# Optimization experiments

Hardware: AMD Instinct MI355X
Metric: run time of the kernel (lower is better)

The kernel has to match this reference:

```python
import jax, jax.numpy as jnp
import numpy as np

B, L, D, H = 2, 128, 256, 256
BASE_LR = 0.01
LR_SHIFT = float(np.log(np.expm1(BASE_LR)))  # log(expm1(base_lr))


def silu_backward(x):
    s = jax.nn.silu(x)
    return s + jax.nn.sigmoid(x) * (1.0 - s)


def decay_matrix(log_g):
    # log_g: [B,L] -> M[b,l,m] = exp(sum_{i=m+1..l} log_g[b,i]) for m<=l, else 0
    n = log_g.shape[1]
    strict = jnp.tril(jnp.ones((n, n), log_g.dtype), -1)
    cum = jnp.cumsum(log_g[:, :, None] * strict, axis=1)
    return jnp.exp(cum) * jnp.tril(jnp.ones((n, n), log_g.dtype))


def setup_inputs():
    key = jax.random.key(0)
    ks = jax.random.split(key, 22)
    p = lambda k, shape: jax.random.normal(k, shape, jnp.float32) * 0.02
    inp = {
        'x': jax.random.normal(ks[0], (B, L, D), jnp.float32),
        'Wq': p(ks[1], (D, D)), 'bq': p(ks[2], (D,)),
        'Wk': p(ks[3], (D, D)), 'bk': p(ks[4], (D,)),
        'Wv': p(ks[5], (D, D)), 'bv': p(ks[6], (D,)),
        'Wlr': p(ks[7], (D, 1)), 'blr': p(ks[8], (1,)),
        'Wm': p(ks[9], (D, 1)), 'bm': p(ks[10], (1,)),
        'Wd': p(ks[11], (D, 1)), 'bd': p(ks[12], (1,)),
        'W1': p(ks[13], (B, H, D)), 'b1': p(ks[14], (B, H)),
        'W2': p(ks[15], (B, D, H)), 'b2': p(ks[16], (B, D)),
        'mW1': p(ks[17], (B, H, D)), 'mb1': p(ks[18], (B, H)),
        'mW2': p(ks[19], (B, D, H)), 'mb2': p(ks[20], (B, D)),
    }
    return inp


def reference(x, Wq, bq, Wk, bk, Wv, bv, Wlr, blr, Wm, bm, Wd, bd,
              W1, b1, W2, b2, mW1, mb1, mW2, mb2):
    query = x @ Wq + bq
    key_ = x @ Wk + bk
    value = x @ Wv + bv

    # forward through fast-weight MLP at current (chunk-start) weights
    Z1 = jnp.einsum('bhd,bld->blh', W1, key_) + b1[:, None, :]
    X2 = jax.nn.silu(Z1)
    Z2 = jnp.einsum('bdh,blh->bld', W2, X2) + b2[:, None, :]

    # per-token gradients of 0.5*||Z2 - value||^2
    grad_Z2 = Z2 - value
    grad_b2 = grad_Z2
    grad_W2 = jnp.einsum('bld,blh->bldh', grad_Z2, X2)
    grad_X2 = jnp.einsum('bld,bdh->blh', grad_Z2, W2)
    grad_Z1 = grad_X2 * silu_backward(Z1)
    grad_b1 = grad_Z1
    grad_W1 = jnp.einsum('blh,bld->blhd', grad_Z1, key_)

    lr = jax.nn.softplus((x @ Wlr).squeeze(-1) + blr + LR_SHIFT)  # [B,L]
    gW1 = grad_W1 * lr[:, :, None, None]
    gb1 = grad_b1 * lr[:, :, None]
    gW2 = grad_W2 * lr[:, :, None, None]
    gb2 = grad_b2 * lr[:, :, None]

    # momentum recurrence (decay-gated linear scan, materialized as LxL matrix)
    fc_mom = (x @ Wm).squeeze(-1) + bm  # [B,L]
    log_mom = -jax.nn.softplus(-fc_mom)
    M = decay_matrix(log_mom)  # [B,L,L]
    mom_cum = jnp.exp(jnp.cumsum(log_mom, axis=1))  # [B,L]

    mgW1 = jnp.einsum('blm,bmhd->blhd', M, gW1) - jnp.einsum('bl,bhd->blhd', mom_cum, mW1)
    mgb1 = jnp.einsum('blm,bmh->blh', M, gb1) - jnp.einsum('bl,bh->blh', mom_cum, mb1)
    mgW2 = jnp.einsum('blm,bmdh->bldh', M, gW2) - jnp.einsum('bl,bdh->bldh', mom_cum, mW2)
    mgb2 = jnp.einsum('blm,bmd->bld', M, gb2) - jnp.einsum('bl,bd->bld', mom_cum, mb2)

    # weight-decay recurrence
    log_wd = -jax.nn.softplus((x @ Wd).squeeze(-1) + bd)  # [B,L]
    Dm = decay_matrix(log_wd)
    wd_cum = jnp.exp(jnp.cumsum(log_wd, axis=1))

    W1p = jnp.einsum('blm,bmhd->blhd', Dm, mgW1) + jnp.einsum('bl,bhd->blhd', wd_cum, W1)
    b1p = jnp.einsum('blm,bmh->blh', Dm, mgb1) + jnp.einsum('bl,bh->blh', wd_cum, b1)
    W2p = jnp.einsum('blm,bmdh->bldh', Dm, mgW2) + jnp.einsum('bl,bdh->bldh', wd_cum, W2)
    b2p = jnp.einsum('blm,bmd->bld', Dm, mgb2) + jnp.einsum('bl,bd->bld', wd_cum, b2)

    # query pass through per-token updated weights
    Zq1 = jnp.einsum('blhd,bld->blh', W1p, query) + b1p
    Zq2 = jnp.einsum('bldh,blh->bld', W2p, jax.nn.silu(Zq1)) + b2p

    return (Zq2,
            W1p[:, -1], b1p[:, -1], W2p[:, -1], b2p[:, -1],
            mgW1[:, -1], mgb1[:, -1], mgW2[:, -1], mgb2[:, -1])
```

## Files before the change

### kernel.cpp

```cpp
#include <hip/hip_runtime.h>
#include <math.h>

constexpr int Bn = 2, Ln = 128, Dn = 256, Hn = 256;

#define LR_SHIFT (-4.6001660040607144f)

constexpr int OFF_Q      = 0;
constexpr int OFF_K      = 65536;
constexpr int OFF_V      = 131072;
constexpr int OFF_X2     = 196608;
constexpr int OFF_GZ1    = 262144;
constexpr int OFF_GZ2    = 327680;
constexpr int OFF_XQ     = 393216;
constexpr int OFF_KT     = 458752;
constexpr int OFF_A      = 524288;
constexpr int OFF_W1T    = 557056;
constexpr int OFF_W2T    = 688128;
constexpr int OFF_MW1T   = 819200;
constexpr int OFF_MW2T   = 950272;
constexpr int OFF_LR     = 1081344;
constexpr int OFF_PM     = 1081600;
constexpr int OFF_PD     = 1081856;
constexpr int OFF_MOMCUM = 1082112;
constexpr int OFF_WDCUM  = 1082368;
constexpr int OFF_C      = 1082624;
constexpr int OFF_LOGM   = 1082880;
constexpr int OFF_LOGWD  = 1083136;
constexpr int OFF_X2T    = 1083392;
constexpr int OFF_U1     = 1148928;
constexpr int OFF_V1     = 1214464;
constexpr int OFF_P1     = 1411072;

constexpr int OUT_ZQ2  = 0;
constexpr int OUT_W1P  = 65536;
constexpr int OUT_B1P  = 196608;
constexpr int OUT_W2P  = 197120;
constexpr int OUT_B2P  = 328192;
constexpr int OUT_MGW1 = 328704;
constexpr int OUT_MGB1 = 459776;
constexpr int OUT_MGW2 = 460288;
constexpr int OUT_MGB2 = 591360;

struct KParams {
    const float *x;
    const float *Wq, *bq, *Wk, *bk, *Wv, *bv;
    const float *Wlr, *blr, *Wm, *bm, *Wd, *bd;
    const float *W1, *b1, *W2, *b2, *mW1, *mb1, *mW2, *mb2;
    float *out, *ws;
};

__device__ __forceinline__ float softplus_f(float z) {
    return fmaxf(z, 0.0f) + log1pf(expf(-fabsf(z)));
}
__device__ __forceinline__ float4 fma4(float s, const float4 w, float4 a) {
    a.x += s * w.x; a.y += s * w.y; a.z += s * w.z; a.w += s * w.w; return a;
}
__device__ __forceinline__ float silu_f(float z) {
    return z / (1.0f + expf(-z));
}
__device__ __forceinline__ float dsilu_mul(float a, float z) {
    float sg = 1.0f / (1.0f + expf(-z));
    return a * (sg * (1.0f + z * (1.0f - sg)));
}

__device__ __forceinline__ void stage8(const float* __restrict__ src,
                                       float (*xs)[260], int t) {
#pragma unroll
    for (int i = 0; i < 2; ++i) {
        int e = t + i * 256; int tok = e >> 6, kq = e & 63;
        *(float4*)&xs[tok][kq * 4] = *(const float4*)(src + tok * 256 + kq * 4);
    }
}

__device__ __forceinline__ float4 dot256(const float (*xs)[260], int tok,
                                         const float* __restrict__ Wc, int ldw) {
    float4 a = {0, 0, 0, 0};
    for (int k0 = 0; k0 < 256; k0 += 16) {
        float4 wb[16];
#pragma unroll
        for (int kk = 0; kk < 16; ++kk)
            wb[kk] = *(const float4*)(Wc + (k0 + kk) * ldw);
#pragma unroll
        for (int kk = 0; kk < 16; ++kk)
            a = fma4(xs[tok][k0 + kk], wb[kk], a);
    }
    return a;
}

__device__ __forceinline__ void lastw_unit(const KParams& p, float* smem, int t,
                                           int b, int fam, int i0, int j0) {
    const float* ws = p.ws;
    float* wa = smem;
    float* wm = smem + 128;
    float (*LA)[16] = (float (*)[16])(smem + 256);
    float (*LM)[16] = (float (*)[16])(smem + 256 + 2048);
    float (*R)[16]  = (float (*)[16])(smem + 256 + 4096);
    const float* lr = ws + OFF_LR + b * Ln;
    const float* Pm = ws + OFF_PM + b * Ln;
    const float* Arow = ws + OFF_A + (b * Ln + Ln - 1) * Ln;
    if (t < 128) {
        wa[t] = Arow[t] * lr[t];
        wm[t] = expf(Pm[Ln - 1] - Pm[t]) * lr[t];
    }
    const float* left  = ws + (fam == 0 ? OFF_GZ1 : OFF_GZ2) + b * Ln * 256;
    const float* right = ws + (fam == 0 ? OFF_K   : OFF_X2 ) + b * Ln * 256;
    __syncthreads();
#pragma unroll
    for (int i = 0; i < 2; ++i) {
        int e = t + i * 256;
        int m = e >> 2, iq = (e & 3) * 4;
        float4 lv = *(const float4*)(left + m * 256 + i0 + iq);
        float4 rv = *(const float4*)(right + m * 256 + j0 + iq);
        float wam = wa[m], wmm = wm[m];
        LA[m][iq + 0] = wam * lv.x; LA[m][iq + 1] = wam * lv.y;
        LA[m][iq + 2] = wam * lv.z; LA[m][iq + 3] = wam * lv.w;
        LM[m][iq + 0] = wmm * lv.x; LM[m][iq + 1] = wmm * lv.y;
        LM[m][iq + 2] = wmm * lv.z; LM[m][iq + 3] = wmm * lv.w;
        R[m][iq + 0] = rv.x; R[m][iq + 1] = rv.y;
        R[m][iq + 2] = rv.z; R[m][iq + 3] = rv.w;
    }
    __syncthreads();
    int tx = t & 15, ty = t >> 4;
    float accA = 0.0f, accM = 0.0f;
#pragma unroll 4
    for (int m = 0; m < 128; ++m) {
        accA += LA[m][ty] * R[m][tx];
        accM += LM[m][ty] * R[m][tx];
    }
    float c_last  = ws[OFF_C + b * Ln + Ln - 1];
    float wd_last = ws[OFF_WDCUM + b * Ln + Ln - 1];
    float mc_last = ws[OFF_MOMCUM + b * Ln + Ln - 1];
    int i = i0 + ty, j = j0 + tx;
    const float* base1 = (fam == 0 ? p.W1 : p.W2) + b * 65536;
    const float* basem = (fam == 0 ? p.mW1 : p.mW2) + b * 65536;
    float b1v = base1[i * 256 + j], bmv = basem[i * 256 + j];
    int op = (fam == 0 ? OUT_W1P : OUT_W2P) + (b * 256 + i) * 256 + j;
    int om = (fam == 0 ? OUT_MGW1 : OUT_MGW2) + (b * 256 + i) * 256 + j;
    p.out[op] = accA - c_last * bmv + wd_last * b1v;
    p.out[om] = accM - mc_last * bmv;
}

__device__ __forceinline__ void score_unit(const KParams& p, float* smem, int t,
                                           int b, int l0, int srcoff, int btoff,
                                           int poff) {
    const float* ws = p.ws;
    float (*qs)[260] = (float (*)[260])smem;
    stage8(ws + srcoff + (b * 128 + l0) * 256, qs, t);
    __syncthreads();
    int tok = t >> 5, mq = t & 31, m0 = 4 * mq;
    int l = l0 + tok;
    float4 s = dot256(qs, tok, ws + btoff + b * 32768 + m0, 128);
    float4 A4 = *(const float4*)(ws + OFF_A + (b * 128 + l) * 128 + m0);
    float4 L4 = *(const float4*)(ws + OFF_LR + b * 128 + m0);
    float4 pv;
    pv.x = (m0 + 0 <= l) ? A4.x * L4.x * (1.0f + s.x) : 0.0f;
    pv.y = (m0 + 1 <= l) ? A4.y * L4.y * (1.0f + s.y) : 0.0f;
    pv.z = (m0 + 2 <= l) ? A4.z * L4.z * (1.0f + s.z) : 0.0f;
    pv.w = (m0 + 3 <= l) ? A4.w * L4.w * (1.0f + s.w) : 0.0f;
    *(float4*)(p.ws + poff + b * 16384 + l * 128 + m0) = pv;
}

__device__ __forceinline__ float4 pg_dot(const float* __restrict__ G,
                                         const float* __restrict__ prow,
                                         int mmax) {
    float4 acc = {0, 0, 0, 0};
    int m0 = 0;
    for (; m0 + 16 <= mmax; m0 += 16) {
        float4 gb[16];
#pragma unroll
        for (int kk = 0; kk < 16; ++kk)
            gb[kk] = *(const float4*)(G + (m0 + kk) * 256);
#pragma unroll
        for (int kk = 0; kk < 16; ++kk)
            acc = fma4(prow[m0 + kk], gb[kk], acc);
    }
    for (; m0 < mmax; m0 += 8) {
        float4 gb[8];
#pragma unroll
        for (int kk = 0; kk < 8; ++kk)
            gb[kk] = *(const float4*)(G + (m0 + kk) * 256);
#pragma unroll
        for (int kk = 0; kk < 8; ++kk)
            acc = fma4(prow[m0 + kk], gb[kk], acc);
    }
    return acc;
}

__global__ __launch_bounds__(256) void phase0_kernel(KParams p) {
    __shared__ float smem[4160];
    int u = blockIdx.x, t = threadIdx.x;
    float* ws = p.ws;
    if (u < 512) {
        int z = u >> 6; int mat = z >> 1; int b = z & 1;
        const float* src; float* dst;
        if (mat == 0)      { src = p.W1  + b * 65536; dst = ws + OFF_W1T  + b * 65536; }
        else if (mat == 1) { src = p.W2  + b * 65536; dst = ws + OFF_W2T  + b * 65536; }
        else if (mat == 2) { src = p.mW1 + b * 65536; dst = ws + OFF_MW1T + b * 65536; }
        else               { src = p.mW2 + b * 65536; dst = ws + OFF_MW2T + b * 65536; }
        float (*tile)[33] = (float (*)[33])smem;
        int tx = t & 31, ty = t >> 5;
        int tid = u & 63;
        int r0 = (tid >> 3) * 32, c0 = (tid & 7) * 32;
        for (int i = 0; i < 32; i += 8)
            tile[ty + i][tx] = src[(r0 + ty + i) * 256 + (c0 + tx)];
        __syncthreads();
        for (int i = 0; i < 32; i += 8)
            dst[(c0 + ty + i) * 256 + (r0 + tx)] = tile[tx][ty + i];
    } else if (u < 704) {
        int v = u - 512; int mat = v >> 6; int r = v & 63;
        int ct = r >> 5, tt = r & 31;
        int bl0 = tt * 8, c0 = ct * 128;
        const float* W    = (mat == 0) ? p.Wq : (mat == 1) ? p.Wk : p.Wv;
        const float* bias = (mat == 0) ? p.bq : (mat == 1) ? p.bk : p.bv;
        int outoff = (mat == 0) ? OFF_Q : (mat == 1) ? OFF_K : OFF_V;
        float (*xs)[260] = (float (*)[260])smem;
        stage8(p.x + bl0 * 256, xs, t);
        __syncthreads();
        int tok = t >> 5, q = t & 31;
        int c = c0 + 4 * q;
        float4 a = dot256(xs, tok, W + c, 256);
        float4 bb = *(const float4*)(bias + c);
        a.x += bb.x; a.y += bb.y; a.z += bb.z; a.w += bb.w;
        *(float4*)(ws + outoff + (bl0 + tok) * 256 + c) = a;
        if (mat == 1) {
            int b = bl0 >> 7, l = (bl0 & 127) + tok;
            float* KT = ws + OFF_KT + b * 32768 + l;
            KT[(c + 0) * 128] = a.x; KT[(c + 1) * 128] = a.y;
            KT[(c + 2) * 128] = a.z; KT[(c + 3) * 128] = a.w;
        }
    } else {
        int blk = u - 704;
        int ln = t & 63, wv = t >> 6;
        int bl = blk * 4 + wv;
        float4 xv = *(const float4*)(p.x + bl * 256 + ln * 4);
        float4 wl = *(const float4*)(p.Wlr + ln * 4);
        float4 wm = *(const float4*)(p.Wm + ln * 4);
        float4 wd = *(const float4*)(p.Wd + ln * 4);
        float s1 = xv.x * wl.x + xv.y * wl.y + xv.z * wl.z + xv.w * wl.w;
        float s2 = xv.x * wm.x + xv.y * wm.y + xv.z * wm.z + xv.w * wm.w;
        float s3 = xv.x * wd.x + xv.y * wd.y + xv.z * wd.z + xv.w * wd.w;
#pragma unroll
        for (int off = 32; off > 0; off >>= 1) {
            s1 += __shfl_xor(s1, off);
            s2 += __shfl_xor(s2, off);
            s3 += __shfl_xor(s3, off);
        }
        if (ln == 0) {
            ws[OFF_LR + bl]    = softplus_f(s1 + p.blr[0] + LR_SHIFT);
            ws[OFF_LOGM + bl]  = -softplus_f(-(s2 + p.bm[0]));
            ws[OFF_LOGWD + bl] = -softplus_f(s3 + p.bd[0]);
        }
    }
}

__global__ __launch_bounds__(256) void phase1_kernel(KParams p) {
    __shared__ float smem[4160];
    int u = blockIdx.x, t = threadIdx.x;
    float* ws = p.ws;
    if (u < 64) {
        int tt = u >> 1, ct = u & 1;
        int bl0 = tt * 8, c0 = ct * 128, b = bl0 >> 7;
        float (*xs)[260] = (float (*)[260])smem;
        stage8(ws + OFF_K + bl0 * 256, xs, t);
        __syncthreads();
        int tok = t >> 5, q = t & 31;
        int c = c0 + 4 * q;
        float4 a = dot256(xs, tok, ws + OFF_W1T + b * 65536 + c, 256);
        float4 bb = *(const float4*)(p.b1 + b * 256 + c);
        float4 z = {a.x + bb.x, a.y + bb.y, a.z + bb.z, a.w + bb.w};
        *(float4*)(ws + OFF_GZ1 + (bl0 + tok) * 256 + c) = z;
        float4 s = {silu_f(z.x), silu_f(z.y), silu_f(z.z), silu_f(z.w)};
        *(float4*)(ws + OFF_X2 + (bl0 + tok) * 256 + c) = s;
        int l = (bl0 & 127) + tok;
        float* X2T = ws + OFF_X2T + b * 32768 + l;
        X2T[(c + 0) * 128] = s.x; X2T[(c + 1) * 128] = s.y;
        X2T[(c + 2) * 128] = s.z; X2T[(c + 3) * 128] = s.w;
    } else if (u < 320) {
        int w = u - 64; int b = w >> 7; int l = w & 127;
        float* sm = smem;
        float* sd = smem + 128;
        float* se = smem + 256;
        if (t < 128) {
            sm[t] = ws[OFF_LOGM + b * Ln + t];
            sd[t] = ws[OFF_LOGWD + b * Ln + t];
        }
        __syncthreads();
        for (int off = 1; off < 128; off <<= 1) {
            float am = 0.0f, ad = 0.0f;
            if (t < 128 && t >= off) { am = sm[t - off]; ad = sd[t - off]; }
            __syncthreads();
            if (t < 128) { sm[t] += am; sd[t] += ad; }
            __syncthreads();
        }
        if (l == 0) {
            if (t < 128) {
                float pm = sm[t], pd = sd[t];
                ws[OFF_PM + b * Ln + t] = pm;
                ws[OFF_PD + b * Ln + t] = pd;
                ws[OFF_MOMCUM + b * Ln + t] = expf(pm);
                ws[OFF_WDCUM + b * Ln + t]  = expf(pd);
                se[t] = expf(pm - pd);
            }
            __syncthreads();
            for (int off = 1; off < 128; off <<= 1) {
                float a = 0.0f;
                if (t < 128 && t >= off) a = se[t - off];
                __syncthreads();
                if (t < 128) se[t] += a;
                __syncthreads();
            }
            if (t < 128) ws[OFF_C + b * Ln + t] = expf(sd[t]) * se[t];
        }
        if (t < 128) {
            int m1 = t;
            float a = 0.0f;
            if (m1 <= l) {
                float pdl = sd[l], pmm1 = sm[m1];
                float s = 0.0f;
                for (int m = m1; m <= l; ++m)
                    s += expf((pdl - sd[m]) + (sm[m] - pmm1));
                a = s;
            }
            ws[OFF_A + (b * Ln + l) * Ln + m1] = a;
        }
    } else {
        int w = u - 320; int mat = w >> 6; int r = w & 63;
        int tt = r >> 1, ct = r & 1;
        int bl0 = tt * 8, c0 = ct * 128, b = bl0 >> 7;
        float (*xs)[260] = (float (*)[260])smem;
        stage8(ws + OFF_Q + bl0 * 256, xs, t);
        __syncthreads();
        int tok = t >> 5, q = t & 31;
        int c = c0 + 4 * q;
        const float* W = ws + (mat ? OFF_MW1T : OFF_W1T) + b * 65536 + c;
        const float* bias = (mat ? p.mb1 : p.b1) + b * 256 + c;
        float4 a = dot256(xs, tok, W, 256);
        float4 bb = *(const float4*)bias;
        a.x += bb.x; a.y += bb.y; a.z += bb.z; a.w += bb.w;
        *(float4*)(ws + (mat ? OFF_V1 : OFF_U1) + (bl0 + tok) * 256 + c) = a;
    }
}

__global__ __launch_bounds__(256) void phase2_kernel(KParams p) {
    __shared__ float smem[4160];
    int u = blockIdx.x, t = threadIdx.x;
    float* ws = p.ws;
    if (u < 32) {
        int bl0 = u * 8, b = bl0 >> 7;
        float (*xs)[260] = (float (*)[260])smem;
        float (*gs)[260] = (float (*)[260])(smem + 2080);
        stage8(ws + OFF_X2 + bl0 * 256, xs, t);
        __syncthreads();
        int tok = t >> 5, q = t & 31;
        int c = 4 * q, c2 = c + 128;
        {
            const float* W2t = ws + OFF_W2T + b * 65536;
            float4 a0 = dot256(xs, tok, W2t + c, 256);
            float4 a1 = dot256(xs, tok, W2t + c2, 256);
            float4 bb0 = *(const float4*)(p.b2 + b * 256 + c);
            float4 bb1 = *(const float4*)(p.b2 + b * 256 + c2);
            float4 v0 = *(const float4*)(ws + OFF_V + (bl0 + tok) * 256 + c);
            float4 v1 = *(const float4*)(ws + OFF_V + (bl0 + tok) * 256 + c2);
            float4 g0 = {a0.x + bb0.x - v0.x, a0.y + bb0.y - v0.y,
                         a0.z + bb0.z - v0.z, a0.w + bb0.w - v0.w};
            float4 g1 = {a1.x + bb1.x - v1.x, a1.y + bb1.y - v1.y,
                         a1.z + bb1.z - v1.z, a1.w + bb1.w - v1.w};
            *(float4*)&gs[tok][c]  = g0;
            *(float4*)&gs[tok][c2] = g1;
            *(float4*)(ws + OFF_GZ2 + (bl0 + tok) * 256 + c)  = g0;
            *(float4*)(ws + OFF_GZ2 + (bl0 + tok) * 256 + c2) = g1;
        }
        __syncthreads();
        {
            const float* W2n = p.W2 + b * 65536;
            float4 a0 = dot256(gs, tok, W2n + c, 256);
            float4 a1 = dot256(gs, tok, W2n + c2, 256);
            float4 z0 = *(const float4*)(ws + OFF_GZ1 + (bl0 + tok) * 256 + c);
            float4 z1 = *(const float4*)(ws + OFF_GZ1 + (bl0 + tok) * 256 + c2);
            float4 g0 = {dsilu_mul(a0.x, z0.x), dsilu_mul(a0.y, z0.y),
                         dsilu_mul(a0.z, z0.z), dsilu_mul(a0.w, z0.w)};
            float4 g1 = {dsilu_mul(a1.x, z1.x), dsilu_mul(a1.y, z1.y),
                         dsilu_mul(a1.z, z1.z), dsilu_mul(a1.w, z1.w)};
            *(float4*)(ws + OFF_GZ1 + (bl0 + tok) * 256 + c)  = g0;
            *(float4*)(ws + OFF_GZ1 + (bl0 + tok) * 256 + c2) = g1;
        }
    } else {
        int w = u - 32; int b = w >> 4; int l0 = (w & 15) * 8;
        score_unit(p, smem, t, b, l0, OFF_Q, OFF_KT, OFF_P1);
    }
}

__global__ __launch_bounds__(256) void phase3_kernel(KParams p) {
    __shared__ float smem[6400];
    int u = blockIdx.x, t = threadIdx.x;
    float* ws = p.ws;
    if (u < 32) {
        int b = u >> 4; int l0 = (u & 15) * 8; int bl0 = b * 128 + l0;
        float (*xqs)[260] = (float (*)[260])smem;
        float (*ps)[132]  = (float (*)[132])(smem + 2080);
        {
            int tok = t >> 5, mq = t & 31;
            *(float4*)&ps[tok][mq * 4] =
                *(const float4*)(ws + OFF_P1 + b * 16384 + (l0 + tok) * 128 + mq * 4);
        }
        __syncthreads();
        int tok = t >> 5, q = t & 31;
        int l = l0 + tok;
        float cl  = ws[OFF_C + b * 128 + l];
        float wdc = ws[OFF_WDCUM + b * 128 + l];
        int mmax = l0 + 8;
#pragma unroll
        for (int half = 0; half < 2; ++half) {
            int c = half * 128 + 4 * q;
            float4 acc = pg_dot(ws + OFF_GZ1 + b * 32768 + c, ps[tok], mmax);
            float4 u4 = *(const float4*)(ws + OFF_U1 + (bl0 + tok) * 256 + c);
            float4 v4 = *(const float4*)(ws + OFF_V1 + (bl0 + tok) * 256 + c);
            float4 o;
            o.x = silu_f(acc.x - cl * v4.x + wdc * u4.x);
            o.y = silu_f(acc.y - cl * v4.y + wdc * u4.y);
            o.z = silu_f(acc.z - cl * v4.z + wdc * u4.z);
            o.w = silu_f(acc.w - cl * v4.w + wdc * u4.w);
            *(float4*)&xqs[tok][c] = o;
        }
        __syncthreads();
        {
            int mq = t & 31, m0 = 4 * mq;
            float4 s = dot256(xqs, tok, ws + OFF_X2T + b * 32768 + m0, 128);
            float4 A4 = *(const float4*)(ws + OFF_A + (b * 128 + l) * 128 + m0);
            float4 L4 = *(const float4*)(ws + OFF_LR + b * 128 + m0);
            float4 pv;
            pv.x = (m0 + 0 <= l) ? A4.x * L4.x * (1.0f + s.x) : 0.0f;
            pv.y = (m0 + 1 <= l) ? A4.y * L4.y * (1.0f + s.y) : 0.0f;
            pv.z = (m0 + 2 <= l) ? A4.z * L4.z * (1.0f + s.z) : 0.0f;
            pv.w = (m0 + 3 <= l) ? A4.w * L4.w * (1.0f + s.w) : 0.0f;
            *(float4*)&ps[tok][m0] = pv;
        }
        __syncthreads();
#pragma unroll
        for (int half = 0; half < 2; ++half) {
            int c = half * 128 + 4 * q;
            float4 uacc = dot256(xqs, tok, ws + OFF_W2T + b * 65536 + c, 256);
            float4 bb = *(const float4*)(p.b2 + b * 256 + c);
            uacc.x += bb.x; uacc.y += bb.y; uacc.z += bb.z; uacc.w += bb.w;
            float4 vacc = dot256(xqs, tok, ws + OFF_MW2T + b * 65536 + c, 256);
            float4 mb = *(const float4*)(p.mb2 + b * 256 + c);
            vacc.x += mb.x; vacc.y += mb.y; vacc.z += mb.z; vacc.w += mb.w;
            float4 acc = pg_dot(ws + OFF_GZ2 + b * 32768 + c, ps[tok], mmax);
            float4 o;
            o.x = acc.x - cl * vacc.x + wdc * uacc.x;
            o.y = acc.y - cl * vacc.y + wdc * uacc.y;
            o.z = acc.z - cl * vacc.z + wdc * uacc.z;
            o.w = acc.w - cl * vacc.w + wdc * uacc.w;
            *(float4*)(p.out + OUT_ZQ2 + (bl0 + tok) * 256 + c) = o;
        }
    } else if (u < 1056) {
        int w = u - 32; int z = w >> 8; int rem = w & 255;
        int b = z >> 1; int fam = z & 1;
        lastw_unit(p, smem, t, b, fam, (rem >> 4) * 16, (rem & 15) * 16);
    } else {
        int b = u - 1056;
        float* wa = smem;
        float* wm = smem + 128;
        if (t < 128) {
            wa[t] = ws[OFF_A + (b * Ln + Ln - 1) * Ln + t] * ws[OFF_LR + b * Ln + t];
            wm[t] = expf(ws[OFF_PM + b * Ln + Ln - 1] - ws[OFF_PM + b * Ln + t]) *
                    ws[OFF_LR + b * Ln + t];
        }
        __syncthreads();
        const float* gz1 = ws + OFF_GZ1 + b * Ln * 256;
        const float* gz2 = ws + OFF_GZ2 + b * Ln * 256;
        float sA1 = 0, sM1 = 0, sA2 = 0, sM2 = 0;
        for (int m0 = 0; m0 < 128; m0 += 16) {
            float g1b[16], g2b[16];
#pragma unroll
            for (int kk = 0; kk < 16; ++kk) {
                g1b[kk] = gz1[(m0 + kk) * 256 + t];
                g2b[kk] = gz2[(m0 + kk) * 256 + t];
            }
#pragma unroll
            for (int kk = 0; kk < 16; ++kk) {
                float wam = wa[m0 + kk], wmm = wm[m0 + kk];
                sA1 += wam * g1b[kk]; sM1 += wmm * g1b[kk];
                sA2 += wam * g2b[kk]; sM2 += wmm * g2b[kk];
            }
        }
        float c_last  = ws[OFF_C + b * Ln + Ln - 1];
        float wd_last = ws[OFF_WDCUM + b * Ln + Ln - 1];
        float mc_last = ws[OFF_MOMCUM + b * Ln + Ln - 1];
        p.out[OUT_B1P + b * 256 + t]  = sA1 - c_last * p.mb1[b * 256 + t] + wd_last * p.b1[b * 256 + t];
        p.out[OUT_MGB1 + b * 256 + t] = sM1 - mc_last * p.mb1[b * 256 + t];
        p.out[OUT_B2P + b * 256 + t]  = sA2 - c_last * p.mb2[b * 256 + t] + wd_last * p.b2[b * 256 + t];
        p.out[OUT_MGB2 + b * 256 + t] = sM2 - mc_last * p.mb2[b * 256 + t];
    }
}

extern "C" void kernel_launch(void* const* d_in, const int* in_sizes, int n_in,
                              void* d_out, int out_size, void* d_ws, size_t ws_size,
                              hipStream_t stream) {
    KParams p;
    p.x   = (const float*)d_in[0];
    p.Wq  = (const float*)d_in[1];  p.bq  = (const float*)d_in[2];
    p.Wk  = (const float*)d_in[3];  p.bk  = (const float*)d_in[4];
    p.Wv  = (const float*)d_in[5];  p.bv  = (const float*)d_in[6];
    p.Wlr = (const float*)d_in[7];  p.blr = (const float*)d_in[8];
    p.Wm  = (const float*)d_in[9];  p.bm  = (const float*)d_in[10];
    p.Wd  = (const float*)d_in[11]; p.bd  = (const float*)d_in[12];
    p.W1  = (const float*)d_in[13]; p.b1  = (const float*)d_in[14];
    p.W2  = (const float*)d_in[15]; p.b2  = (const float*)d_in[16];
    p.mW1 = (const float*)d_in[17]; p.mb1 = (const float*)d_in[18];
    p.mW2 = (const float*)d_in[19]; p.mb2 = (const float*)d_in[20];
    p.out = (float*)d_out;
    p.ws  = (float*)d_ws;

    phase0_kernel<<<768, 256, 0, stream>>>(p);
    phase1_kernel<<<448, 256, 0, stream>>>(p);
    phase2_kernel<<<64, 256, 0, stream>>>(p);
    phase3_kernel<<<1058, 256, 0, stream>>>(p);
}
```

Measured before the change: 222.4 us.

## Restructure phases: fold scans into phase0, fuse K-projection into MLP, split query pass

```diff
diff --git a/kernel.cpp b/kernel.cpp
--- a/kernel.cpp
+++ b/kernel.cpp
@@ -24,11 +24,11 @@
 constexpr int OFF_MOMCUM = 1082112;
 constexpr int OFF_WDCUM  = 1082368;
 constexpr int OFF_C      = 1082624;
-constexpr int OFF_LOGM   = 1082880;
-constexpr int OFF_LOGWD  = 1083136;
 constexpr int OFF_X2T    = 1083392;
 constexpr int OFF_U1     = 1148928;
 constexpr int OFF_V1     = 1214464;
+constexpr int OFF_U2     = 1280000;
+constexpr int OFF_V2     = 1345536;
 constexpr int OFF_P1     = 1411072;
 
 constexpr int OUT_ZQ2  = 0;
@@ -186,12 +186,118 @@
     return acc;
 }
 
+__device__ __forceinline__ void combine_unit(const KParams& p, float* smem, int t,
+                                             int b, int l0, int c0, int poff,
+                                             int goff, int uoff, int voff,
+                                             int dooutsilu, float* dst) {
+    const float* ws = p.ws;
+    int bl0 = b * 128 + l0;
+    float (*ps)[132] = (float (*)[132])smem;
+    {
+        int tok = t >> 5, mq = t & 31;
+        *(float4*)&ps[tok][mq * 4] =
+            *(const float4*)(ws + poff + b * 16384 + (l0 + tok) * 128 + mq * 4);
+    }
+    __syncthreads();
+    int tok = t >> 5, q = t & 31;
+    int l = l0 + tok;
+    int c = c0 + 4 * q;
+    float cl  = ws[OFF_C + b * 128 + l];
+    float wdc = ws[OFF_WDCUM + b * 128 + l];
+    float4 acc = pg_dot(ws + goff + b * 32768 + c, ps[tok], l0 + 8);
+    float4 u4 = *(const float4*)(ws + uoff + (bl0 + tok) * 256 + c);
+    float4 v4 = *(const float4*)(ws + voff + (bl0 + tok) * 256 + c);
+    float4 o;
+    o.x = acc.x - cl * v4.x + wdc * u4.x;
+    o.y = acc.y - cl * v4.y + wdc * u4.y;
+    o.z = acc.z - cl * v4.z + wdc * u4.z;
+    o.w = acc.w - cl * v4.w + wdc * u4.w;
+    if (dooutsilu) {
+        o.x = silu_f(o.x); o.y = silu_f(o.y); o.z = silu_f(o.z); o.w = silu_f(o.w);
+    }
+    *(float4*)(dst + (bl0 + tok) * 256 + c) = o;
+}
+
 __global__ __launch_bounds__(256) void phase0_kernel(KParams p) {
     __shared__ float smem[4160];
     int u = blockIdx.x, t = threadIdx.x;
     float* ws = p.ws;
-    if (u < 512) {
-        int z = u >> 6; int mat = z >> 1; int b = z & 1;
+    if (u < 2) {
+        int b = u;
+        float* sm = smem;
+        float* sd = smem + 128;
+        float* se = smem + 256;
+        int wv = t >> 6, ln = t & 63;
+        float4 wl = *(const float4*)(p.Wlr + ln * 4);
+        float4 wm = *(const float4*)(p.Wm + ln * 4);
+        float4 wd = *(const float4*)(p.Wd + ln * 4);
+        for (int r = 0; r < 4; ++r) {
+            float4 xr[8];
+#pragma unroll
+            for (int j = 0; j < 8; ++j) {
+                int tok = wv * 32 + r * 8 + j;
+                xr[j] = *(const float4*)(p.x + (b * 128 + tok) * 256 + ln * 4);
+            }
+#pragma unroll
+            for (int j = 0; j < 8; ++j) {
+                int tok = wv * 32 + r * 8 + j;
+                float s1 = xr[j].x * wl.x + xr[j].y * wl.y + xr[j].z * wl.z + xr[j].w * wl.w;
+                float s2 = xr[j].x * wm.x + xr[j].y * wm.y + xr[j].z * wm.z + xr[j].w * wm.w;
+                float s3 = xr[j].x * wd.x + xr[j].y * wd.y + xr[j].z * wd.z + xr[j].w * wd.w;
+#pragma unroll
+                for (int off = 32; off > 0; off >>= 1) {
+                    s1 += __shfl_xor(s1, off);
+                    s2 += __shfl_xor(s2, off);
+                    s3 += __shfl_xor(s3, off);
+                }
+                if (ln == 0) {
+                    ws[OFF_LR + b * 128 + tok] = softplus_f(s1 + p.blr[0] + LR_SHIFT);
+                    sm[tok] = -softplus_f(-(s2 + p.bm[0]));
+                    sd[tok] = -softplus_f(s3 + p.bd[0]);
+                }
+            }
+        }
+        __syncthreads();
+        for (int off = 1; off < 128; off <<= 1) {
+            float am = 0.0f, ad = 0.0f;
+            if (t < 128 && t >= off) { am = sm[t - off]; ad = sd[t - off]; }
+            __syncthreads();
+            if (t < 128) { sm[t] += am; sd[t] += ad; }
+            __syncthreads();
+        }
+        if (t < 128) {
+            float pm = sm[t], pd = sd[t];
+            ws[OFF_PM + b * Ln + t] = pm;
+            ws[OFF_PD + b * Ln + t] = pd;
+            ws[OFF_MOMCUM + b * Ln + t] = expf(pm);
+            ws[OFF_WDCUM + b * Ln + t]  = expf(pd);
+            se[t] = expf(pm - pd);
+        }
+        __syncthreads();
+        for (int off = 1; off < 128; off <<= 1) {
+            float a = 0.0f;
+            if (t < 128 && t >= off) a = se[t - off];
+            __syncthreads();
+            if (t < 128) se[t] += a;
+            __syncthreads();
+        }
+        if (t < 128) ws[OFF_C + b * Ln + t] = expf(sd[t]) * se[t];
+        __syncthreads();
+        for (int e = t; e < 16384; e += 256) {
+            int l = e >> 7, m1 = e & 127;
+            float a = 0.0f;
+            if (m1 <= l) {
+                float pdl = sd[l], pmm1 = sm[m1];
+                float s = 0.0f;
+                for (int m = m1; m <= l; ++m)
+                    s += expf((pdl - sd[m]) + (sm[m] - pmm1));
+                a = s;
+            }
+            ws[OFF_A + (b * Ln + l) * Ln + m1] = a;
+        }
+    } else if (u < 514) {
+        int w = u - 2;
+        int z = w >> 6; int mat = z >> 1; int b = z & 1;
         const float* src; float* dst;
         if (mat == 0)      { src = p.W1  + b * 65536; dst = ws + OFF_W1T  + b * 65536; }
         else if (mat == 1) { src = p.W2  + b * 65536; dst = ws + OFF_W2T  + b * 65536; }
@@ -199,15 +305,15 @@
         else               { src = p.mW2 + b * 65536; dst = ws + OFF_MW2T + b * 65536; }
         float (*tile)[33] = (float (*)[33])smem;
         int tx = t & 31, ty = t >> 5;
-        int tid = u & 63;
+        int tid = w & 63;
         int r0 = (tid >> 3) * 32, c0 = (tid & 7) * 32;
         for (int i = 0; i < 32; i += 8)
             tile[ty + i][tx] = src[(r0 + ty + i) * 256 + (c0 + tx)];
         __syncthreads();
         for (int i = 0; i < 32; i += 8)
             dst[(c0 + ty + i) * 256 + (r0 + tx)] = tile[tx][ty + i];
-    } else if (u < 704) {
-        int v = u - 512; int mat = v >> 6; int r = v & 63;
+    } else {
+        int v = u - 514; int mat = v >> 6; int r = v & 63;
         int ct = r >> 5, tt = r & 31;
         int bl0 = tt * 8, c0 = ct * 128;
         const float* W    = (mat == 0) ? p.Wq : (mat == 1) ? p.Wk : p.Wv;
@@ -228,135 +334,55 @@
             KT[(c + 0) * 128] = a.x; KT[(c + 1) * 128] = a.y;
             KT[(c + 2) * 128] = a.z; KT[(c + 3) * 128] = a.w;
         }
-    } else {
-        int blk = u - 704;
-        int ln = t & 63, wv = t >> 6;
-        int bl = blk * 4 + wv;
-        float4 xv = *(const float4*)(p.x + bl * 256 + ln * 4);
-        float4 wl = *(const float4*)(p.Wlr + ln * 4);
-        float4 wm = *(const float4*)(p.Wm + ln * 4);
-        float4 wd = *(const float4*)(p.Wd + ln * 4);
-        float s1 = xv.x * wl.x + xv.y * wl.y + xv.z * wl.z + xv.w * wl.w;
-        float s2 = xv.x * wm.x + xv.y * wm.y + xv.z * wm.z + xv.w * wm.w;
-        float s3 = xv.x * wd.x + xv.y * wd.y + xv.z * wd.z + xv.w * wd.w;
-#pragma unroll
-        for (int off = 32; off > 0; off >>= 1) {
-            s1 += __shfl_xor(s1, off);
-            s2 += __shfl_xor(s2, off);
-            s3 += __shfl_xor(s3, off);
-        }
-        if (ln == 0) {
-            ws[OFF_LR + bl]    = softplus_f(s1 + p.blr[0] + LR_SHIFT);
-            ws[OFF_LOGM + bl]  = -softplus_f(-(s2 + p.bm[0]));
-            ws[OFF_LOGWD + bl] = -softplus_f(s3 + p.bd[0]);
-        }
     }
 }
 
 __global__ __launch_bounds__(256) void phase1_kernel(KParams p) {
-    __shared__ float smem[4160];
-    int u = blockIdx.x, t = threadIdx.x;
-    float* ws = p.ws;
-    if (u < 64) {
-        int tt = u >> 1, ct = u & 1;
-        int bl0 = tt * 8, c0 = ct * 128, b = bl0 >> 7;
-        float (*xs)[260] = (float (*)[260])smem;
-        stage8(ws + OFF_K + bl0 * 256, xs, t);
-        __syncthreads();
-        int tok = t >> 5, q = t & 31;
-        int c = c0 + 4 * q;
-        float4 a = dot256(xs, tok, ws + OFF_W1T + b * 65536 + c, 256);
-        float4 bb = *(const float4*)(p.b1 + b * 256 + c);
-        float4 z = {a.x + bb.x, a.y + bb.y, a.z + bb.z, a.w + bb.w};
-        *(float4*)(ws + OFF_GZ1 + (bl0 + tok) * 256 + c) = z;
-        float4 s = {silu_f(z.x), silu_f(z.y), silu_f(z.z), silu_f(z.w)};
-        *(float4*)(ws + OFF_X2 + (bl0 + tok) * 256 + c) = s;
-        int l = (bl0 & 127) + tok;
-        float* X2T = ws + OFF_X2T + b * 32768 + l;
-        X2T[(c + 0) * 128] = s.x; X2T[(c + 1) * 128] = s.y;
-        X2T[(c + 2) * 128] = s.z; X2T[(c + 3) * 128] = s.w;
-    } else if (u < 320) {
-        int w = u - 64; int b = w >> 7; int l = w & 127;
-        float* sm = smem;
-        float* sd = smem + 128;
-        float* se = smem + 256;
-        if (t < 128) {
-            sm[t] = ws[OFF_LOGM + b * Ln + t];
-            sd[t] = ws[OFF_LOGWD + b * Ln + t];
-        }
-        __syncthreads();
-        for (int off = 1; off < 128; off <<= 1) {
-            float am = 0.0f, ad = 0.0f;
-            if (t < 128 && t >= off) { am = sm[t - off]; ad = sd[t - off]; }
-            __syncthreads();
-            if (t < 128) { sm[t] += am; sd[t] += ad; }
-            __syncthreads();
-        }
-        if (l == 0) {
-            if (t < 128) {
-                float pm = sm[t], pd = sd[t];
-                ws[OFF_PM + b * Ln + t] = pm;
-                ws[OFF_PD + b * Ln + t] = pd;
-                ws[OFF_MOMCUM + b * Ln + t] = expf(pm);
-                ws[OFF_WDCUM + b * Ln + t]  = expf(pd);
-                se[t] = expf(pm - pd);
-            }
-            __syncthreads();
-            for (int off = 1; off < 128; off <<= 1) {
-                float a = 0.0f;
-                if (t < 128 && t >= off) a = se[t - off];
-                __syncthreads();
-                if (t < 128) se[t] += a;
-                __syncthreads();
-            }
-            if (t < 128) ws[OFF_C + b * Ln + t] = expf(sd[t]) * se[t];
-        }
-        if (t < 128) {
-            int m1 = t;
-            float a = 0.0f;
-            if (m1 <= l) {
-                float pdl = sd[l], pmm1 = sm[m1];
-                float s = 0.0f;
-                for (int m = m1; m <= l; ++m)
-                    s += expf((pdl - sd[m]) + (sm[m] - pmm1));
-                a = s;
-            }
-            ws[OFF_A + (b * Ln + l) * Ln + m1] = a;
-        }
-    } else {
-        int w = u - 320; int mat = w >> 6; int r = w & 63;
-        int tt = r >> 1, ct = r & 1;
-        int bl0 = tt * 8, c0 = ct * 128, b = bl0 >> 7;
-        float (*xs)[260] = (float (*)[260])smem;
-        stage8(ws + OFF_Q + bl0 * 256, xs, t);
-        __syncthreads();
-        int tok = t >> 5, q = t & 31;
-        int c = c0 + 4 * q;
-        const float* W = ws + (mat ? OFF_MW1T : OFF_W1T) + b * 65536 + c;
-        const float* bias = (mat ? p.mb1 : p.b1) + b * 256 + c;
-        float4 a = dot256(xs, tok, W, 256);
-        float4 bb = *(const float4*)bias;
-        a.x += bb.x; a.y += bb.y; a.z += bb.z; a.w += bb.w;
-        *(float4*)(ws + (mat ? OFF_V1 : OFF_U1) + (bl0 + tok) * 256 + c) = a;
-    }
-}
-
-__global__ __launch_bounds__(256) void phase2_kernel(KParams p) {
-    __shared__ float smem[4160];
+    __shared__ float smem[8320];
     int u = blockIdx.x, t = threadIdx.x;
     float* ws = p.ws;
     if (u < 32) {
         int bl0 = u * 8, b = bl0 >> 7;
-        float (*xs)[260] = (float (*)[260])smem;
-        float (*gs)[260] = (float (*)[260])(smem + 2080);
-        stage8(ws + OFF_X2 + bl0 * 256, xs, t);
+        float (*ks)[260] = (float (*)[260])smem;
+        float (*zs)[260] = (float (*)[260])(smem + 2080);
+        float (*as)[260] = (float (*)[260])(smem + 4160);
+        float (*gs)[260] = (float (*)[260])(smem + 6240);
+        stage8(ws + OFF_K + bl0 * 256, ks, t);
         __syncthreads();
         int tok = t >> 5, q = t & 31;
         int c = 4 * q, c2 = c + 128;
         {
+            const float* W1t = ws + OFF_W1T + b * 65536;
+            float4 a0 = dot256(ks, tok, W1t + c, 256);
+            float4 a1 = dot256(ks, tok, W1t + c2, 256);
+            float4 bb0 = *(const float4*)(p.b1 + b * 256 + c);
+            float4 bb1 = *(const float4*)(p.b1 + b * 256 + c2);
+            float4 z0 = {a0.x + bb0.x, a0.y + bb0.y, a0.z + bb0.z, a0.w + bb0.w};
+            float4 z1 = {a1.x + bb1.x, a1.y + bb1.y, a1.z + bb1.z, a1.w + bb1.w};
+            *(float4*)&zs[tok][c]  = z0;
+            *(float4*)&zs[tok][c2] = z1;
+            float4 s0 = {silu_f(z0.x), silu_f(z0.y), silu_f(z0.z), silu_f(z0.w)};
+            float4 s1 = {silu_f(z1.x), silu_f(z1.y), silu_f(z1.z), silu_f(z1.w)};
+            *(float4*)&as[tok][c]  = s0;
+            *(float4*)&as[tok][c2] = s1;
+            *(float4*)(ws + OFF_X2 + (bl0 + tok) * 256 + c)  = s0;
+            *(float4*)(ws + OFF_X2 + (bl0 + tok) * 256 + c2) = s1;
+        }
+        __syncthreads();
+        {
+            int l0b = bl0 & 127;
+            float v1[8];
+#pragma unroll
+            for (int j = 0; j < 8; ++j) v1[j] = as[j][t];
+            float* X2Tp = ws + OFF_X2T + b * 32768 + t * 128 + l0b;
+            float4 r0 = {v1[0], v1[1], v1[2], v1[3]};
+            float4 r1 = {v1[4], v1[5], v1[6], v1[7]};
+            *(float4*)X2Tp = r0; *(float4*)(X2Tp + 4) = r1;
+        }
+        {
             const float* W2t = ws + OFF_W2T + b * 65536;
-            float4 a0 = dot256(xs, tok, W2t + c, 256);
-            float4 a1 = dot256(xs, tok, W2t + c2, 256);
+            float4 a0 = dot256(as, tok, W2t + c, 256);
+            float4 a1 = dot256(as, tok, W2t + c2, 256);
             float4 bb0 = *(const float4*)(p.b2 + b * 256 + c);
             float4 bb1 = *(const float4*)(p.b2 + b * 256 + c2);
             float4 v0 = *(const float4*)(ws + OFF_V + (bl0 + tok) * 256 + c);
@@ -375,8 +401,8 @@
             const float* W2n = p.W2 + b * 65536;
             float4 a0 = dot256(gs, tok, W2n + c, 256);
             float4 a1 = dot256(gs, tok, W2n + c2, 256);
-            float4 z0 = *(const float4*)(ws + OFF_GZ1 + (bl0 + tok) * 256 + c);
-            float4 z1 = *(const float4*)(ws + OFF_GZ1 + (bl0 + tok) * 256 + c2);
+            float4 z0 = *(float4*)&zs[tok][c];
+            float4 z1 = *(float4*)&zs[tok][c2];
             float4 g0 = {dsilu_mul(a0.x, z0.x), dsilu_mul(a0.y, z0.y),
                          dsilu_mul(a0.z, z0.z), dsilu_mul(a0.w, z0.w)};
             float4 g1 = {dsilu_mul(a1.x, z1.x), dsilu_mul(a1.y, z1.y),
@@ -384,81 +410,42 @@
             *(float4*)(ws + OFF_GZ1 + (bl0 + tok) * 256 + c)  = g0;
             *(float4*)(ws + OFF_GZ1 + (bl0 + tok) * 256 + c2) = g1;
         }
+    } else if (u < 160) {
+        int w = u - 32; int mat = w >> 6; int r = w & 63;
+        int tt = r >> 1, ct = r & 1;
+        int bl0 = tt * 8, c0 = ct * 128, b = bl0 >> 7;
+        float (*xs)[260] = (float (*)[260])smem;
+        stage8(ws + OFF_Q + bl0 * 256, xs, t);
+        __syncthreads();
+        int tok = t >> 5, q = t & 31;
+        int c = c0 + 4 * q;
+        const float* W = ws + (mat ? OFF_MW1T : OFF_W1T) + b * 65536 + c;
+        const float* bias = (mat ? p.mb1 : p.b1) + b * 256 + c;
+        float4 a = dot256(xs, tok, W, 256);
+        float4 bb = *(const float4*)bias;
+        a.x += bb.x; a.y += bb.y; a.z += bb.z; a.w += bb.w;
+        *(float4*)(ws + (mat ? OFF_V1 : OFF_U1) + (bl0 + tok) * 256 + c) = a;
     } else {
-        int w = u - 32; int b = w >> 4; int l0 = (w & 15) * 8;
+        int w = u - 160; int b = w >> 4; int l0 = (w & 15) * 8;
         score_unit(p, smem, t, b, l0, OFF_Q, OFF_KT, OFF_P1);
     }
 }
 
-__global__ __launch_bounds__(256) void phase3_kernel(KParams p) {
+__global__ __launch_bounds__(256) void phase2_kernel(KParams p) {
     __shared__ float smem[6400];
     int u = blockIdx.x, t = threadIdx.x;
     float* ws = p.ws;
-    if (u < 32) {
-        int b = u >> 4; int l0 = (u & 15) * 8; int bl0 = b * 128 + l0;
-        float (*xqs)[260] = (float (*)[260])smem;
-        float (*ps)[132]  = (float (*)[132])(smem + 2080);
-        {
-            int tok = t >> 5, mq = t & 31;
-            *(float4*)&ps[tok][mq * 4] =
-                *(const float4*)(ws + OFF_P1 + b * 16384 + (l0 + tok) * 128 + mq * 4);
-        }
-        __syncthreads();
-        int tok = t >> 5, q = t & 31;
-        int l = l0 + tok;
-        float cl  = ws[OFF_C + b * 128 + l];
-        float wdc = ws[OFF_WDCUM + b * 128 + l];
-        int mmax = l0 + 8;
-#pragma unroll
-        for (int half = 0; half < 2; ++half) {
-            int c = half * 128 + 4 * q;
-            float4 acc = pg_dot(ws + OFF_GZ1 + b * 32768 + c, ps[tok], mmax);
-            float4 u4 = *(const float4*)(ws + OFF_U1 + (bl0 + tok) * 256 + c);
-            float4 v4 = *(const float4*)(ws + OFF_V1 + (bl0 + tok) * 256 + c);
-            float4 o;
-            o.x = silu_f(acc.x - cl * v4.x + wdc * u4.x);
-            o.y = silu_f(acc.y - cl * v4.y + wdc * u4.y);
-            o.z = silu_f(acc.z - cl * v4.z + wdc * u4.z);
-            o.w = silu_f(acc.w - cl * v4.w + wdc * u4.w);
-            *(float4*)&xqs[tok][c] = o;
-        }
-        __syncthreads();
-        {
-            int mq = t & 31, m0 = 4 * mq;
-            float4 s = dot256(xqs, tok, ws + OFF_X2T + b * 32768 + m0, 128);
-            float4 A4 = *(const float4*)(ws + OFF_A + (b * 128 + l) * 128 + m0);
-            float4 L4 = *(const float4*)(ws + OFF_LR + b * 128 + m0);
-            float4 pv;
-            pv.x = (m0 + 0 <= l) ? A4.x * L4.x * (1.0f + s.x) : 0.0f;
-            pv.y = (m0 + 1 <= l) ? A4.y * L4.y * (1.0f + s.y) : 0.0f;
-            pv.z = (m0 + 2 <= l) ? A4.z * L4.z * (1.0f + s.z) : 0.0f;
-            pv.w = (m0 + 3 <= l) ? A4.w * L4.w * (1.0f + s.w) : 0.0f;
-            *(float4*)&ps[tok][m0] = pv;
-        }
-        __syncthreads();
-#pragma unroll
-        for (int half = 0; half < 2; ++half) {
-            int c = half * 128 + 4 * q;
-            float4 uacc = dot256(xqs, tok, ws + OFF_W2T + b * 65536 + c, 256);
-            float4 bb = *(const float4*)(p.b2 + b * 256 + c);
-            uacc.x += bb.x; uacc.y += bb.y; uacc.z += bb.z; uacc.w += bb.w;
-            float4 vacc = dot256(xqs, tok, ws + OFF_MW2T + b * 65536 + c, 256);
-            float4 mb = *(const float4*)(p.mb2 + b * 256 + c);
-            vacc.x += mb.x; vacc.y += mb.y; vacc.z += mb.z; vacc.w += mb.w;
-            float4 acc = pg_dot(ws + OFF_GZ2 + b * 32768 + c, ps[tok], mmax);
-            float4 o;
-            o.x = acc.x - cl * vacc.x + wdc * uacc.x;
-            o.y = acc.y - cl * vacc.y + wdc * uacc.y;
-            o.z = acc.z - cl * vacc.z + wdc * uacc.z;
-            o.w = acc.w - cl * vacc.w + wdc * uacc.w;
-            *(float4*)(p.out + OUT_ZQ2 + (bl0 + tok) * 256 + c) = o;
-        }
-    } else if (u < 1056) {
-        int w = u - 32; int z = w >> 8; int rem = w & 255;
+    if (u < 64) {
+        int tt = u >> 1, ct = u & 1;
+        int b = tt >> 4, l0 = (tt & 15) * 8;
+        combine_unit(p, smem, t, b, l0, ct * 128, OFF_P1, OFF_GZ1,
+                     OFF_U1, OFF_V1, 1, ws + OFF_XQ);
+    } else if (u < 1088) {
+        int w = u - 64; int z = w >> 8; int rem = w & 255;
         int b = z >> 1; int fam = z & 1;
         lastw_unit(p, smem, t, b, fam, (rem >> 4) * 16, (rem & 15) * 16);
     } else {
-        int b = u - 1056;
+        int b = u - 1088;
         float* wa = smem;
         float* wm = smem + 128;
         if (t < 128) {
@@ -492,6 +479,40 @@
         p.out[OUT_B2P + b * 256 + t]  = sA2 - c_last * p.mb2[b * 256 + t] + wd_last * p.b2[b * 256 + t];
         p.out[OUT_MGB2 + b * 256 + t] = sM2 - mc_last * p.mb2[b * 256 + t];
     }
+}
+
+__global__ __launch_bounds__(256) void phase3_kernel(KParams p) {
+    __shared__ float smem[4160];
+    int u = blockIdx.x, t = threadIdx.x;
+    float* ws = p.ws;
+    if (u < 32) {
+        int b = u >> 4; int l0 = (u & 15) * 8;
+        score_unit(p, smem, t, b, l0, OFF_XQ, OFF_X2T, OFF_P1);
+    } else {
+        int w = u - 32; int mat = w >> 6; int r = w & 63;
+        int tt = r >> 1, ct = r & 1;
+        int bl0 = tt * 8, c0 = ct * 128, b = bl0 >> 7;
+        float (*xs)[260] = (float (*)[260])smem;
+        stage8(ws + OFF_XQ + bl0 * 256, xs, t);
+        __syncthreads();
+        int tok = t >> 5, q = t & 31;
+        int c = c0 + 4 * q;
+        const float* W = ws + (mat ? OFF_MW2T : OFF_W2T) + b * 65536 + c;
+        const float* bias = (mat ? p.mb2 : p.b2) + b * 256 + c;
+        float4 a = dot256(xs, tok, W, 256);
+        float4 bb = *(const float4*)bias;
+        a.x += bb.x; a.y += bb.y; a.z += bb.z; a.w += bb.w;
+        *(float4*)(ws + (mat ? OFF_V2 : OFF_U2) + (bl0 + tok) * 256 + c) = a;
+    }
+}
+
+__global__ __launch_bounds__(256) void phase4_kernel(KParams p) {
+    __shared__ float smem[1056];
+    int u = blockIdx.x, t = threadIdx.x;
+    int tt = u >> 1, ct = u & 1;
+    int b = tt >> 4, l0 = (tt & 15) * 8;
+    combine_unit(p, smem, t, b, l0, ct * 128, OFF_P1, OFF_GZ2,
+                 OFF_U2, OFF_V2, 0, p.out + OUT_ZQ2);
 }
 
 extern "C" void kernel_launch(void* const* d_in, const int* in_sizes, int n_in,
@@ -512,8 +533,9 @@
     p.out = (float*)d_out;
     p.ws  = (float*)d_ws;
 
-    phase0_kernel<<<768, 256, 0, stream>>>(p);
-    phase1_kernel<<<448, 256, 0, stream>>>(p);
-    phase2_kernel<<<64, 256, 0, stream>>>(p);
-    phase3_kernel<<<1058, 256, 0, stream>>>(p);
-}
+    phase0_kernel<<<706, 256, 0, stream>>>(p);
+    phase1_kernel<<<192, 256, 0, stream>>>(p);
+    phase2_kernel<<<1090, 256, 0, stream>>>(p);
+    phase3_kernel<<<160, 256, 0, stream>>>(p);
+    phase4_kernel<<<64, 256, 0, stream>>>(p);
+}
```

After: 563.8 us. 2.54x slower.
